# Kernel optimization log

Measured on AMD Instinct MI355X. Metric: run time of the kernel, lower is better.

The kernel has to match this reference:

```python
import jax, jax.numpy as jnp
import numpy as np

HEADS = 6
EPS = 1e-5


def _na_idx(L, k, d):
    # NATTEN-style dilated neighborhood: work within dilation cosets,
    # clamp window to stay inside the image (window shifts at borders).
    i = np.arange(L)
    g = i % d
    p = i // d
    Lg = (L - g + d - 1) // d  # coset length per position
    start = np.clip(p - k // 2, 0, Lg - k)
    j = np.arange(k)
    nbr = g[:, None] + d * (start[:, None] + j[None, :])          # [L,k] neighbor coords
    rel = (start[:, None] + j[None, :]) - p[:, None] + (k - 1)    # [L,k] rpb index in [0,2k-2]
    return jnp.asarray(nbr, jnp.int32), jnp.asarray(rel, jnp.int32)


def _na2d(x, qkv_w, qkv_b, proj_w, proj_b, rpb, heads, k, d):
    # x: [B,H,W,C] NHWC neighborhood attention with relative positional bias
    B, H, W, C = x.shape
    dh = C // heads
    scale = dh ** -0.5
    qkv = (x @ qkv_w + qkv_b).reshape(B, H, W, 3, heads, dh)
    qkv = jnp.transpose(qkv, (3, 0, 4, 1, 2, 5))  # [3,B,h,H,W,dh]
    q, kk, v = qkv[0] * scale, qkv[1], qkv[2]
    nh, rh = _na_idx(H, k, d)
    nw, rw = _na_idx(W, k, d)

    def gather(t):  # [B,h,H,W,dh] -> [B,h,H,W,k,k,dh]
        t = t[:, :, nh]              # [B,h,H,k,W,dh]
        t = t[:, :, :, :, nw]        # [B,h,H,k,W,k,dh]
        return jnp.transpose(t, (0, 1, 2, 4, 3, 5, 6))

    kn, vn = gather(kk), gather(v)
    attn = jnp.einsum('bhxyd,bhxyijd->bhxyij', q, kn)  # [B,h,H,W,k,k]
    bias = rpb[:, rh]                  # [h,H,k,2k-1]
    bias = bias[:, :, :, rw]           # [h,H,k,W,k]
    bias = jnp.transpose(bias, (0, 1, 3, 2, 4))  # [h,H,W,k,k]
    attn = attn + bias[None]
    attn = jax.nn.softmax(attn.reshape(B, heads, H, W, k * k), axis=-1)
    attn = attn.reshape(B, heads, H, W, k, k)
    out = jnp.einsum('bhxyij,bhxyijd->bhxyd', attn, vn)
    out = jnp.transpose(out, (0, 2, 3, 1, 4)).reshape(B, H, W, C)
    return out @ proj_w + proj_b


def _rln(x, w, b, m1_w, m1_b, m2_w, m2_b):
    # Revised LayerNorm: normalize over (C,H,W) per sample; meta1/meta2 are 1x1 convs on std/mean
    mean = jnp.mean(x, axis=(1, 2, 3), keepdims=True)
    std = jnp.sqrt(jnp.mean((x - mean) ** 2, axis=(1, 2, 3), keepdims=True) + EPS)
    out = (x - mean) / std * w + b
    rescale = m1_w[None, :, None, None] * std + m1_b[None, :, None, None]
    rebias = m2_w[None, :, None, None] * mean + m2_b[None, :, None, None]
    return out, rescale, rebias


def _c11(x, w, b):  # 1x1 conv on NCHW == per-pixel linear
    return jnp.einsum('bchw,oc->bohw', x, w) + b[None, :, None, None]


def _gelu(x):
    return jax.nn.gelu(x, approximate=False)


def reference(x, ln_w, ln_b, m1_w, m1_b, m2_w, m2_b, qkv1_w, qkv1_b, proj1_w, proj1_b, rpb1, qkv2_w, qkv2_b, proj2_w, proj2_b, rpb2, mlp_w1, mlp_b1, mlp_w2, mlp_b2, bn_g, bn_b, bn_m, bn_v, pa_w1, pa_b1, pa_w2, pa_b2, ca_w1, ca_b1, ca_w2, ca_b2, m2a_w1, m2a_b1, m2a_w2, m2a_b2):
    # ---- NA block 1 (kernel 7, dilation 1) ----
    sc = x
    y, rs, rb = _rln(x, ln_w, ln_b, m1_w, m1_b, m2_w, m2_b)
    a = _na2d(jnp.transpose(y, (0, 2, 3, 1)), qkv1_w, qkv1_b, proj1_w, proj1_b, rpb1, HEADS, 7, 1)
    x = sc + jnp.transpose(a, (0, 3, 1, 2)) * rs + rb
    # ---- NA block 2 (kernel 5, dilation 8) ----
    sc = x
    y, rs, rb = _rln(x, ln_w, ln_b, m1_w, m1_b, m2_w, m2_b)
    a = _na2d(jnp.transpose(y, (0, 2, 3, 1)), qkv2_w, qkv2_b, proj2_w, proj2_b, rpb2, HEADS, 5, 8)
    x = sc + jnp.transpose(a, (0, 3, 1, 2)) * rs + rb
    # ---- MLP (source reuses the pre-attn2 shortcut `sc`) ----
    y, rs, rb = _rln(x, ln_w, ln_b, m1_w, m1_b, m2_w, m2_b)
    m = _c11(jax.nn.relu(_c11(y, mlp_w1, mlp_b1)), mlp_w2, mlp_b2)
    x = sc + m * rs + rb
    # ---- BN + pixel attention + channel attention + mlp2 ----
    sc = x
    inv = jax.lax.rsqrt(bn_v + EPS)
    y = (x - bn_m[None, :, None, None]) * (inv * bn_g)[None, :, None, None] + bn_b[None, :, None, None]
    pa = jax.nn.sigmoid(_c11(_gelu(_c11(y, pa_w1, pa_b1)), pa_w2, pa_b2))  # [B,1,H,W]
    y = pa * y
    gap = jnp.mean(y, axis=(2, 3), keepdims=True)
    ca = jax.nn.sigmoid(_c11(_gelu(_c11(gap, ca_w1, ca_b1)), ca_w2, ca_b2))  # [B,C,1,1]
    y = ca * y
    y = _c11(_gelu(_c11(y, m2a_w1, m2a_b1)), m2a_w2, m2a_b2)
    return sc + y


def setup_inputs() -> dict:
    key = jax.random.key(0)
    B, C, H, W, HID = 4, 96, 64, 64, 384
    ks = iter(jax.random.split(key, 48))

    def rn(shape, s=0.02):
        return jax.random.normal(next(ks), shape, jnp.float32) * s

    d = {}
    d['x'] = jax.random.normal(next(ks), (B, C, H, W), jnp.float32)
    d['ln_w'] = jnp.ones((1, C, 1, 1), jnp.float32)
    d['ln_b'] = jnp.zeros((1, C, 1, 1), jnp.float32)
    d['m1_w'] = rn((C,)); d['m1_b'] = jnp.ones((C,), jnp.float32)
    d['m2_w'] = rn((C,)); d['m2_b'] = jnp.zeros((C,), jnp.float32)
    d['qkv1_w'] = rn((C, 3 * C)); d['qkv1_b'] = jnp.zeros((3 * C,), jnp.float32)
    d['proj1_w'] = rn((C, C)); d['proj1_b'] = jnp.zeros((C,), jnp.float32)
    d['rpb1'] = rn((HEADS, 13, 13))
    d['qkv2_w'] = rn((C, 3 * C)); d['qkv2_b'] = jnp.zeros((3 * C,), jnp.float32)
    d['proj2_w'] = rn((C, C)); d['proj2_b'] = jnp.zeros((C,), jnp.float32)
    d['rpb2'] = rn((HEADS, 9, 9))
    d['mlp_w1'] = rn((HID, C)); d['mlp_b1'] = jnp.zeros((HID,), jnp.float32)
    d['mlp_w2'] = rn((C, HID)); d['mlp_b2'] = jnp.zeros((C,), jnp.float32)
    d['bn_g'] = jnp.ones((C,), jnp.float32); d['bn_b'] = jnp.zeros((C,), jnp.float32)
    d['bn_m'] = jnp.zeros((C,), jnp.float32); d['bn_v'] = jnp.ones((C,), jnp.float32)
    d['pa_w1'] = rn((C // 8, C)); d['pa_b1'] = jnp.zeros((C // 8,), jnp.float32)
    d['pa_w2'] = rn((1, C // 8)); d['pa_b2'] = jnp.zeros((1,), jnp.float32)
    d['ca_w1'] = rn((C, C)); d['ca_b1'] = jnp.zeros((C,), jnp.float32)
    d['ca_w2'] = rn((C, C)); d['ca_b2'] = jnp.zeros((C,), jnp.float32)
    d['m2a_w1'] = rn((C, C)); d['m2a_b1'] = jnp.zeros((C,), jnp.float32)
    d['m2a_w2'] = rn((C, C)); d['m2a_b2'] = jnp.zeros((C,), jnp.float32)
    return d
```

## Files before the change

kernel.cpp:

```cpp
#include <hip/hip_runtime.h>
#include <math.h>

#define CC 96
#define NP 4096
#define NHEADS 6
#define NELEMF 393216.0f
#define EPSF 1e-5f

typedef __attribute__((ext_vector_type(8))) short bf16x8;
typedef __attribute__((ext_vector_type(4))) float f32x4;
#define MFMA16(a,b,c) __builtin_amdgcn_mfma_f32_16x16x32_bf16(a,b,c,0,0,0)

#define WQKV1  64
#define WQKV2  (WQKV1+13824)
#define WPROJ1 (WQKV2+13824)
#define WPROJ2 (WPROJ1+4608)
#define WMLP1  (WPROJ2+4608)
#define WMLP2  (WMLP1+18432)
#define WM2A1  (WMLP2+18432)
#define WM2A2  (WM2A1+4608)
#define WPA1T  (WM2A2+4608)
#define WBNS   (WPA1T+1152)
#define WCA1T  (WBNS+192)
#define WCA2T  (WCA1T+9216)
#define WS_Q   870784
#define WS_K   (WS_Q+786432)
#define WS_V   (WS_K+786432)
#define WS_ATTPM (WS_V+786432)
#define WS_X1  (WS_ATTPM+786432)
#define WS_X2  (WS_X1+1572864)
#define WS_X3  (WS_X2+1572864)
#define WS_PA  (WS_X3+1572864)
#define WS_GAP (WS_PA+16384)

__device__ __forceinline__ float gelu_f(float x){
  return 0.5f * x * (1.0f + erff(x * 0.7071067811865476f));
}
__device__ __forceinline__ float sigmoid_f(float x){
  return 1.0f / (1.0f + __expf(-x));
}
__device__ __forceinline__ unsigned short bfr(float f){
  unsigned int u = __float_as_uint(f);
  u += 0x7fffu + ((u >> 16) & 1u);
  return (unsigned short)(u >> 16);
}
__device__ __forceinline__ float bflo16(unsigned short u){ return __uint_as_float(((unsigned int)u) << 16); }
__device__ __forceinline__ float bflo(unsigned int u){ return __uint_as_float(u << 16); }
__device__ __forceinline__ float bfhi(unsigned int u){ return __uint_as_float(u & 0xffff0000u); }
__device__ __forceinline__ void get_ms(const float* st, int b, float& mean, float& inv, float& stdv){
  float s = st[b], s2 = st[4+b];
  mean = s * (1.0f/NELEMF);
  float var = fmaxf(s2 * (1.0f/NELEMF) - mean*mean, 0.0f);
  stdv = sqrtf(var + EPSF);
  inv = 1.0f / stdv;
}
__device__ __forceinline__ float ldf(const float* p, int i){ return p[i]; }
__device__ __forceinline__ float ldf(const unsigned short* p, int i){ return bflo16(p[i]); }
__device__ __forceinline__ void load4(const float* p, float4& v){ v = *(const float4*)p; }
__device__ __forceinline__ void load4(const unsigned short* p, float4& v){
  ushort4 u = *(const ushort4*)p;
  v.x = bflo16(u.x); v.y = bflo16(u.y); v.z = bflo16(u.z); v.w = bflo16(u.w);
}

__device__ __forceinline__ float dotg(const float* qv, const uint4* p){
  uint4 a = p[0], b = p[1];
  float s;
  s  = qv[0]*bflo(a.x);            s = fmaf(qv[1],  bfhi(a.x), s);
  s = fmaf(qv[2],  bflo(a.y), s);  s = fmaf(qv[3],  bfhi(a.y), s);
  s = fmaf(qv[4],  bflo(a.z), s);  s = fmaf(qv[5],  bfhi(a.z), s);
  s = fmaf(qv[6],  bflo(a.w), s);  s = fmaf(qv[7],  bfhi(a.w), s);
  s = fmaf(qv[8],  bflo(b.x), s);  s = fmaf(qv[9],  bfhi(b.x), s);
  s = fmaf(qv[10], bflo(b.y), s);  s = fmaf(qv[11], bfhi(b.y), s);
  s = fmaf(qv[12], bflo(b.z), s);  s = fmaf(qv[13], bfhi(b.z), s);
  s = fmaf(qv[14], bflo(b.w), s);  s = fmaf(qv[15], bfhi(b.w), s);
  return s;
}
__device__ __forceinline__ void pvg(float w, const uint4* p, float* acc){
  uint4 a = p[0], b = p[1];
  acc[0]  = fmaf(w, bflo(a.x), acc[0]);  acc[1]  = fmaf(w, bfhi(a.x), acc[1]);
  acc[2]  = fmaf(w, bflo(a.y), acc[2]);  acc[3]  = fmaf(w, bfhi(a.y), acc[3]);
  acc[4]  = fmaf(w, bflo(a.z), acc[4]);  acc[5]  = fmaf(w, bfhi(a.z), acc[5]);
  acc[6]  = fmaf(w, bflo(a.w), acc[6]);  acc[7]  = fmaf(w, bfhi(a.w), acc[7]);
  acc[8]  = fmaf(w, bflo(b.x), acc[8]);  acc[9]  = fmaf(w, bfhi(b.x), acc[9]);
  acc[10] = fmaf(w, bflo(b.y), acc[10]); acc[11] = fmaf(w, bfhi(b.y), acc[11]);
  acc[12] = fmaf(w, bflo(b.z), acc[12]); acc[13] = fmaf(w, bfhi(b.z), acc[13]);
  acc[14] = fmaf(w, bflo(b.w), acc[14]); acc[15] = fmaf(w, bfhi(b.w), acc[15]);
}

__global__ void prep_stats_kernel(const float* __restrict__ x, float* __restrict__ st,
                             const float* __restrict__ q1, const float* __restrict__ q2,
                             const float* __restrict__ p1, const float* __restrict__ p2,
                             const float* __restrict__ w1, const float* __restrict__ w2,
                             const float* __restrict__ a1, const float* __restrict__ a2,
                             const float* __restrict__ pw1,
                             const float* __restrict__ bg, const float* __restrict__ bb,
                             const float* __restrict__ bm, const float* __restrict__ bv,
                             const float* __restrict__ cw1, const float* __restrict__ cw2,
                             float* __restrict__ ws){
  if(blockIdx.x < 384){
    int b = blockIdx.x / CC, c = blockIdx.x % CC;
    const float4* p4 = (const float4*)(x + (size_t)(b*CC + c)*NP);
    float s = 0.f, s2 = 0.f;
    for(int i = threadIdx.x; i < 1024; i += 256){
      float4 v = p4[i];
      s += v.x + v.y + v.z + v.w;
      s2 = fmaf(v.x, v.x, fmaf(v.y, v.y, fmaf(v.z, v.z, fmaf(v.w, v.w, s2))));
    }
    for(int off = 32; off > 0; off >>= 1){ s += __shfl_down(s, off); s2 += __shfl_down(s2, off); }
    __shared__ float ls[8];
    int wid = threadIdx.x >> 6;
    if((threadIdx.x & 63) == 0){ ls[wid] = s; ls[4+wid] = s2; }
    __syncthreads();
    if(threadIdx.x == 0){
      atomicAdd(&st[b],   ls[0]+ls[1]+ls[2]+ls[3]);
      atomicAdd(&st[4+b], ls[4]+ls[5]+ls[6]+ls[7]);
    }
    return;
  }
  int gid = (blockIdx.x - 384)*256 + threadIdx.x;
  if(gid < 27648){ int n = gid/96, c = gid%96; ((unsigned short*)(ws+WQKV1))[gid] = bfr(q1[c*288+n]); }
  else if(gid < 55296){ int g = gid-27648; int n = g/96, c = g%96; ((unsigned short*)(ws+WQKV2))[g] = bfr(q2[c*288+n]); }
  else if(gid < 64512){ int g = gid-55296; int n = g/96, c = g%96; ((unsigned short*)(ws+WPROJ1))[g] = bfr(p1[c*96+n]); }
  else if(gid < 73728){ int g = gid-64512; int n = g/96, c = g%96; ((unsigned short*)(ws+WPROJ2))[g] = bfr(p2[c*96+n]); }
  else if(gid < 110592){ int g = gid-73728; ((unsigned short*)(ws+WMLP1))[g] = bfr(w1[g]); }
  else if(gid < 147456){ int g = gid-110592; ((unsigned short*)(ws+WMLP2))[g] = bfr(w2[g]); }
  else if(gid < 156672){ int g = gid-147456; ((unsigned short*)(ws+WM2A1))[g] = bfr(a1[g]); }
  else if(gid < 165888){ int g = gid-156672; ((unsigned short*)(ws+WM2A2))[g] = bfr(a2[g]); }
  else if(gid < 167040){ int g = gid-165888; int c = g/12, h = g%12; ws[WPA1T + g] = pw1[h*96+c]; }
  else if(gid < 167136){ int c = gid-167040;
    float sc = rsqrtf(bv[c] + EPSF) * bg[c];
    ws[WBNS + c] = sc;
    ws[WBNS + 96 + c] = bb[c] - bm[c]*sc;
  }
  else if(gid < 167520){ ws[WS_GAP + (gid-167136)] = 0.f; }
  else if(gid < 176736){ int g = gid-167520; int o = g/96, c = g%96; ws[WCA1T + c*96 + o] = cw1[g]; }
  else if(gid < 185952){ int g = gid-176736; int o = g/96, c = g%96; ws[WCA2T + c*96 + o] = cw2[g]; }
}

template<typename AT>
__global__ void __launch_bounds__(512) gemm_qkv_kernel(
    const AT* __restrict__ xin, const float* __restrict__ st,
    const float* __restrict__ lnw, const float* __restrict__ lnb,
    const unsigned short* __restrict__ wT, const float* __restrict__ qb,
    unsigned short* __restrict__ qo, unsigned short* __restrict__ ko, unsigned short* __restrict__ vo){
  __shared__ unsigned short Atl[64*104];
  __shared__ float scl[96], ofs[96];
  int m_base = blockIdx.x*64;
  int b = m_base >> 12, pxl0 = m_base & 4095;
  float mean, inv, stdv; get_ms(st, b, mean, inv, stdv);
  int tid = threadIdx.x;
  if(tid < 96){ float s = inv*lnw[tid]; scl[tid] = s; ofs[tid] = lnb[tid] - mean*s; }
  __syncthreads();
  const AT* src = xin + (size_t)b*CC*NP + pxl0;
  for(int idx = tid; idx < 96*16; idx += 512){
    int c = idx >> 4, p4 = (idx & 15) << 2;
    float4 v; load4(src + (size_t)c*NP + p4, v);
    float s = scl[c], o = ofs[c];
    Atl[(p4+0)*104 + c] = bfr(fmaf(v.x, s, o));
    Atl[(p4+1)*104 + c] = bfr(fmaf(v.y, s, o));
    Atl[(p4+2)*104 + c] = bfr(fmaf(v.z, s, o));
    Atl[(p4+3)*104 + c] = bfr(fmaf(v.w, s, o));
  }
  __syncthreads();
  int w = tid >> 6, lane = tid & 63, ml = lane & 15, q = lane >> 4;
  int row = w & 3, nh = w >> 2;
  const unsigned short* arow = Atl + (row*16 + ml)*104;
  bf16x8 av[3];
  #pragma unroll
  for(int ks = 0; ks < 3; ++ks) av[ks] = *(const bf16x8*)(arow + ks*32 + q*8);
  f32x4 z = {0.f,0.f,0.f,0.f};
  #pragma unroll
  for(int g0 = 0; g0 < 3; ++g0){
    int g = nh*3 + g0;
    f32x4 acc[3] = {z, z, z};
    #pragma unroll
    for(int ks = 0; ks < 3; ++ks){
      #pragma unroll
      for(int gg = 0; gg < 3; ++gg){
        bf16x8 bv = *(const bf16x8*)(wT + (g*48 + gg*16 + ml)*96 + ks*32 + q*8);
        acc[gg] = MFMA16(av[ks], bv, acc[gg]);
      }
    }
    #pragma unroll
    for(int gg = 0; gg < 3; ++gg){
      int nfb = g*48 + gg*16;
      int t = nfb/96, head = (nfb%96) >> 4;
      float scale = (t == 0) ? 0.25f : 1.0f;
      unsigned short* dst = (t == 0) ? qo : (t == 1) ? ko : vo;
      float bias = qb[nfb + ml];
      #pragma unroll
      for(int r = 0; r < 4; ++r){
        int pxl = pxl0 + row*16 + q*4 + r;
        dst[(((size_t)(b*NHEADS + head))*NP + pxl)*16 + ml] = bfr((acc[gg][r] + bias)*scale);
      }
    }
  }
}

template<int K, int D, int RPB, typename SCT>
__global__ void __launch_bounds__(512) attnproj_kernel(
    const unsigned short* __restrict__ qb, const unsigned short* __restrict__ kb,
    const unsigned short* __restrict__ vb, const float* __restrict__ rpb,
    const unsigned short* __restrict__ wT, const float* __restrict__ pb,
    const SCT* __restrict__ scx, const float* __restrict__ st,
    const float* __restrict__ m1w, const float* __restrict__ m1b,
    const float* __restrict__ m2w, const float* __restrict__ m2b,
    unsigned short* __restrict__ dst, float* __restrict__ st_out){
  __shared__ __align__(16) char smbuf[26624];
  __shared__ float rpbl[NHEADS*RPB*RPB];
  __shared__ float ls[16];
  unsigned short* attout = (unsigned short*)smbuf;
  float* T = (float*)smbuf;
  int b = blockIdx.x >> 6;
  int x = blockIdx.x & 63;
  int tid = threadIdx.x;
  for(int i = tid; i < NHEADS*RPB*RPB; i += 512) rpbl[i] = rpb[i];
  __syncthreads();

  if(tid < 384){
    int head = tid >> 6;
    int y = tid & 63;
    int bh = b*NHEADS + head;
    int gx = (D == 1) ? 0 : (x & (D-1));
    int px = (D == 1) ? x : (x >> 3);
    int Lgx = (64 - gx + D - 1) / D;
    int sx = min(max(px - K/2, 0), Lgx - K);
    int gy = (D == 1) ? 0 : (y & (D-1));
    int py = (D == 1) ? y : (y >> 3);
    int Lgy = (64 - gy + D - 1) / D;
    int sy = min(max(py - K/2, 0), Lgy - K);
    int dxb = sx - px + (K-1);
    int dyb = sy - py + (K-1);
    int pix = x*64 + y;

    float qv[16];
    {
      const uint4* qg = (const uint4*)(qb + ((size_t)bh*NP + pix)*16);
      uint4 qa = qg[0], qb4 = qg[1];
      qv[0]=bflo(qa.x);  qv[1]=bfhi(qa.x);  qv[2]=bflo(qa.y);  qv[3]=bfhi(qa.y);
      qv[4]=bflo(qa.z);  qv[5]=bfhi(qa.z);  qv[6]=bflo(qa.w);  qv[7]=bfhi(qa.w);
      qv[8]=bflo(qb4.x); qv[9]=bfhi(qb4.x); qv[10]=bflo(qb4.y);qv[11]=bfhi(qb4.y);
      qv[12]=bflo(qb4.z);qv[13]=bfhi(qb4.z);qv[14]=bflo(qb4.w);qv[15]=bfhi(qb4.w);
    }
    const unsigned short* kgb = kb + (size_t)bh*NP*16;
    const unsigned short* vgb = vb + (size_t)bh*NP*16;

    float sc[K*K];
    #pragma unroll
    for(int i = 0; i < K; ++i){
      int colx = gx + D*(sx + i);
      const unsigned short* kcol = kgb + (size_t)colx*64*16;
      const float* br = rpbl + (head*RPB + (i + dxb))*RPB + dyb;
      #pragma unroll
      for(int j = 0; j < K; ++j){
        int wwy = gy + D*(sy + j);
        sc[i*K + j] = dotg(qv, (const uint4*)(kcol + wwy*16)) + br[j];
      }
    }
    float mx = -1e30f;
    #pragma unroll
    for(int n = 0; n < K*K; ++n) mx = fmaxf(mx, sc[n]);
    float sum = 0.f;
    #pragma unroll
    for(int n = 0; n < K*K; ++n){ float e = __expf(sc[n] - mx); sc[n] = e; sum += e; }
    float rs = 1.0f / sum;
    float acc[16];
    #pragma unroll
    for(int d = 0; d < 16; ++d) acc[d] = 0.f;
    #pragma unroll
    for(int i = 0; i < K; ++i){
      int colx = gx + D*(sx + i);
      const unsigned short* vcol = vgb + (size_t)colx*64*16;
      #pragma unroll
      for(int j = 0; j < K; ++j){
        int wwy = gy + D*(sy + j);
        pvg(sc[i*K + j] * rs, (const uint4*)(vcol + wwy*16), acc);
      }
    }
    unsigned int ow[8];
    #pragma unroll
    for(int p = 0; p < 8; ++p)
      ow[p] = (unsigned int)bfr(acc[2*p]) | ((unsigned int)bfr(acc[2*p+1]) << 16);
    unsigned short* op = attout + y*104 + head*16;
    *(uint4*)op = make_uint4(ow[0], ow[1], ow[2], ow[3]);
    *(uint4*)(op + 8) = make_uint4(ow[4], ow[5], ow[6], ow[7]);
  }
  __syncthreads();

  int w = tid >> 6, lane = tid & 63, ml = lane & 15, q = lane >> 4;
  int row = w & 3, nh = w >> 2;
  f32x4 z = {0.f,0.f,0.f,0.f};
  f32x4 acc[3] = {z, z, z};
  {
    const unsigned short* arow = attout + (row*16 + ml)*104;
    #pragma unroll
    for(int ks = 0; ks < 3; ++ks){
      bf16x8 av = *(const bf16x8*)(arow + ks*32 + q*8);
      #pragma unroll
      for(int g0 = 0; g0 < 3; ++g0){
        int g = nh*3 + g0;
        bf16x8 bv = *(const bf16x8*)(wT + (g*16 + ml)*96 + ks*32 + q*8);
        acc[g0] = MFMA16(av, bv, acc[g0]);
      }
    }
  }
  __syncthreads();
  #pragma unroll
  for(int g0 = 0; g0 < 3; ++g0){
    int g = nh*3 + g0;
    #pragma unroll
    for(int r = 0; r < 4; ++r)
      T[(g*16 + ml)*68 + row*16 + q*4 + r] = acc[g0][r];
  }
  __syncthreads();
  int pxl0 = x*64;
  float mean, inv, stdv; get_ms(st, b, mean, inv, stdv);
  float s = 0.f, s2 = 0.f;
  for(int idx = tid; idx < 96*64; idx += 512){
    int n = idx >> 6, p = idx & 63;
    float rsf = fmaf(m1w[n], stdv, m1b[n]);
    float rbf = fmaf(m2w[n], mean, m2b[n]);
    int ad = (b*CC + n)*NP + pxl0 + p;
    float val = ldf(scx, ad) + (T[n*68 + p] + pb[n])*rsf + rbf;
    dst[ad] = bfr(val);
    s += val; s2 = fmaf(val, val, s2);
  }
  for(int off = 32; off > 0; off >>= 1){ s += __shfl_down(s, off); s2 += __shfl_down(s2, off); }
  if(lane == 0){ ls[w] = s; ls[8+w] = s2; }
  __syncthreads();
  if(tid == 0){
    float a0 = 0.f, a1 = 0.f;
    #pragma unroll
    for(int i = 0; i < 8; ++i){ a0 += ls[i]; a1 += ls[8+i]; }
    atomicAdd(&st_out[b], a0);
    atomicAdd(&st_out[4+b], a1);
  }
}

__global__ void __launch_bounds__(512) gemm_mlp_kernel(
    const unsigned short* __restrict__ xin, const float* __restrict__ st,
    const float* __restrict__ lnw, const float* __restrict__ lnb,
    const unsigned short* __restrict__ w1T, const float* __restrict__ b1,
    const unsigned short* __restrict__ w2T, const float* __restrict__ b2,
    const unsigned short* __restrict__ scx,
    const float* __restrict__ m1w, const float* __restrict__ m1b,
    const float* __restrict__ m2w, const float* __restrict__ m2b,
    float* __restrict__ dst,
    const float* __restrict__ bns, const float* __restrict__ pw1t,
    const float* __restrict__ pb1, const float* __restrict__ pw2,
    const float* __restrict__ pb2, float* __restrict__ pa,
    float* __restrict__ gap){
  __shared__ __align__(16) char smbuf[63488];
  __shared__ float scl[96], ofs[96];
  unsigned short* Atl  = (unsigned short*)smbuf;
  unsigned short* hidL = (unsigned short*)(smbuf + 13312);
  float* T = (float*)(smbuf + 13312);
  float* gpart = (float*)smbuf;
  int m_base = blockIdx.x*64;
  int b = m_base >> 12, pxl0 = m_base & 4095;
  float mean, inv, stdv; get_ms(st, b, mean, inv, stdv);
  int tid = threadIdx.x;
  if(tid < 96){ float s = inv*lnw[tid]; scl[tid] = s; ofs[tid] = lnb[tid] - mean*s; }
  __syncthreads();
  const unsigned short* src = xin + (size_t)b*CC*NP + pxl0;
  for(int idx = tid; idx < 96*16; idx += 512){
    int c = idx >> 4, p4 = (idx & 15) << 2;
    float4 v; load4(src + (size_t)c*NP + p4, v);
    float s = scl[c], o = ofs[c];
    Atl[(p4+0)*104 + c] = bfr(fmaf(v.x, s, o));
    Atl[(p4+1)*104 + c] = bfr(fmaf(v.y, s, o));
    Atl[(p4+2)*104 + c] = bfr(fmaf(v.z, s, o));
    Atl[(p4+3)*104 + c] = bfr(fmaf(v.w, s, o));
  }
  __syncthreads();
  int w = tid >> 6, lane = tid & 63, ml = lane & 15, q = lane >> 4;
  int row = w & 3, nh = w >> 2;
  f32x4 z = {0.f,0.f,0.f,0.f};
  {
    const unsigned short* arow = Atl + (row*16 + ml)*104;
    bf16x8 av[3];
    #pragma unroll
    for(int ks = 0; ks < 3; ++ks) av[ks] = *(const bf16x8*)(arow + ks*32 + q*8);
    #pragma unroll
    for(int g0 = 0; g0 < 4; ++g0){
      int g = nh*4 + g0;
      f32x4 acc[3] = {z, z, z};
      #pragma unroll
      for(int ks = 0; ks < 3; ++ks){
        #pragma unroll
        for(int gg = 0; gg < 3; ++gg){
          bf16x8 bv = *(const bf16x8*)(w1T + (g*48 + gg*16 + ml)*96 + ks*32 + q*8);
          acc[gg] = MFMA16(av[ks], bv, acc[gg]);
        }
      }
      #pragma unroll
      for(int gg = 0; gg < 3; ++gg){
        int n = g*48 + gg*16 + ml;
        float bias = b1[n];
        #pragma unroll
        for(int r = 0; r < 4; ++r)
          hidL[(row*16 + q*4 + r)*392 + n] = bfr(fmaxf(acc[gg][r] + bias, 0.f));
      }
    }
  }
  __syncthreads();
  f32x4 acc2[3] = {z, z, z};
  {
    const unsigned short* arow = hidL + (row*16 + ml)*392;
    #pragma unroll
    for(int ks = 0; ks < 12; ++ks){
      bf16x8 av = *(const bf16x8*)(arow + ks*32 + q*8);
      #pragma unroll
      for(int g0 = 0; g0 < 3; ++g0){
        int g = nh*3 + g0;
        bf16x8 bv = *(const bf16x8*)(w2T + (g*16 + ml)*384 + ks*32 + q*8);
        acc2[g0] = MFMA16(av, bv, acc2[g0]);
      }
    }
  }
  __syncthreads();
  #pragma unroll
  for(int g0 = 0; g0 < 3; ++g0){
    int g = nh*3 + g0;
    #pragma unroll
    for(int r = 0; r < 4; ++r)
      T[(g*16 + ml)*68 + row*16 + q*4 + r] = acc2[g0][r];
  }
  __syncthreads();
  for(int idx = tid; idx < 96*64; idx += 512){
    int n = idx >> 6, px = idx & 63;
    float rsf = fmaf(m1w[n], stdv, m1b[n]);
    float rbf = fmaf(m2w[n], mean, m2b[n]);
    int ad = (b*CC + n)*NP + pxl0 + px;
    float val = ldf(scx, ad) + (T[n*68 + px] + b2[n])*rsf + rbf;
    dst[ad] = val;
    T[n*68 + px] = val;
  }
  __syncthreads();
  int pxq = tid >> 3, t = tid & 7;
  float yvv[12], acc[12];
  #pragma unroll
  for(int h = 0; h < 12; ++h) acc[h] = 0.f;
  #pragma unroll 6
  for(int cc = 0; cc < 12; ++cc){
    int c = t*12 + cc;
    float yv = fmaf(T[c*68 + pxq], bns[c], bns[96 + c]);
    yvv[cc] = yv;
    #pragma unroll
    for(int h = 0; h < 12; ++h) acc[h] = fmaf(yv, pw1t[c*12 + h], acc[h]);
  }
  #pragma unroll
  for(int h = 0; h < 12; ++h){
    acc[h] += __shfl_xor(acc[h], 1);
    acc[h] += __shfl_xor(acc[h], 2);
    acc[h] += __shfl_xor(acc[h], 4);
  }
  float s = pb2[0];
  #pragma unroll
  for(int h = 0; h < 12; ++h) s = fmaf(gelu_f(acc[h] + pb1[h]), pw2[h], s);
  float pav = sigmoid_f(s);
  if(t == 0) pa[b*NP + pxl0 + pxq] = pav;
  #pragma unroll 6
  for(int cc = 0; cc < 12; ++cc){
    float g = yvv[cc] * pav;
    g += __shfl_xor(g, 8);  g += __shfl_xor(g, 16); g += __shfl_xor(g, 32);
    if(lane < 8) gpart[w*96 + lane*12 + cc] = g;
  }
  __syncthreads();
  if(tid < 96){
    int c = tid;
    float v = 0.f;
    #pragma unroll
    for(int ww = 0; ww < 8; ++ww) v += gpart[ww*96 + c];
    atomicAdd(&gap[b*96 + c], v * (1.0f/4096.0f));
  }
}

__global__ void __launch_bounds__(512) gemm_m2a_kernel(
    const float* __restrict__ x3, const float* __restrict__ bns,
    const float* __restrict__ pa, const float* __restrict__ gap,
    const float* __restrict__ cw1T, const float* __restrict__ cb1,
    const float* __restrict__ cw2T, const float* __restrict__ cb2,
    const unsigned short* __restrict__ w1T, const float* __restrict__ b1,
    const unsigned short* __restrict__ w2T, const float* __restrict__ b2,
    const float* __restrict__ scx, float* __restrict__ outp){
  __shared__ __align__(16) char smbuf[26624];
  __shared__ float scl[96], ofs[96], pal[64];
  __shared__ float gl[96], tl[96];
  unsigned short* Atl = (unsigned short*)smbuf;
  unsigned short* tl2 = (unsigned short*)(smbuf + 13312);
  float* T = (float*)smbuf;
  int m_base = blockIdx.x*64;
  int b = m_base >> 12, pxl0 = m_base & 4095;
  int tid = threadIdx.x;
  if(tid < 96) gl[tid] = gap[b*96 + tid];
  if(tid >= 128 && tid < 192) pal[tid-128] = pa[m_base + (tid-128)];
  __syncthreads();
  if(tid < 96){
    float a = cb1[tid];
    #pragma unroll 8
    for(int c = 0; c < 96; ++c) a = fmaf(gl[c], cw1T[c*96 + tid], a);
    tl[tid] = gelu_f(a);
  }
  __syncthreads();
  if(tid < 96){
    float a = cb2[tid];
    #pragma unroll 8
    for(int c = 0; c < 96; ++c) a = fmaf(tl[c], cw2T[c*96 + tid], a);
    float cv = sigmoid_f(a);
    scl[tid] = bns[tid]*cv; ofs[tid] = bns[96+tid]*cv;
  }
  __syncthreads();
  const float* src = x3 + (size_t)b*CC*NP + pxl0;
  for(int idx = tid; idx < 96*16; idx += 512){
    int c = idx >> 4, p4 = (idx & 15) << 2;
    float4 v = *(const float4*)(src + (size_t)c*NP + p4);
    float s = scl[c], o = ofs[c];
    Atl[(p4+0)*104 + c] = bfr(fmaf(v.x, s, o) * pal[p4+0]);
    Atl[(p4+1)*104 + c] = bfr(fmaf(v.y, s, o) * pal[p4+1]);
    Atl[(p4+2)*104 + c] = bfr(fmaf(v.z, s, o) * pal[p4+2]);
    Atl[(p4+3)*104 + c] = bfr(fmaf(v.w, s, o) * pal[p4+3]);
  }
  __syncthreads();
  int w = tid >> 6, lane = tid & 63, ml = lane & 15, q = lane >> 4;
  int row = w & 3, nh = w >> 2;
  f32x4 z = {0.f,0.f,0.f,0.f};
  f32x4 acc1[3] = {z, z, z};
  {
    const unsigned short* arow = Atl + (row*16 + ml)*104;
    #pragma unroll
    for(int ks = 0; ks < 3; ++ks){
      bf16x8 av = *(const bf16x8*)(arow + ks*32 + q*8);
      #pragma unroll
      for(int g0 = 0; g0 < 3; ++g0){
        int g = nh*3 + g0;
        bf16x8 bv = *(const bf16x8*)(w1T + (g*16 + ml)*96 + ks*32 + q*8);
        acc1[g0] = MFMA16(av, bv, acc1[g0]);
      }
    }
  }
  #pragma unroll
  for(int g0 = 0; g0 < 3; ++g0){
    int g = nh*3 + g0;
    float bias = b1[g*16 + ml];
    #pragma unroll
    for(int r = 0; r < 4; ++r)
      tl2[(row*16 + q*4 + r)*104 + g*16 + ml] = bfr(gelu_f(acc1[g0][r] + bias));
  }
  __syncthreads();
  f32x4 acc2[3] = {z, z, z};
  {
    const unsigned short* arow = tl2 + (row*16 + ml)*104;
    #pragma unroll
    for(int ks = 0; ks < 3; ++ks){
      bf16x8 av = *(const bf16x8*)(arow + ks*32 + q*8);
      #pragma unroll
      for(int g0 = 0; g0 < 3; ++g0){
        int g = nh*3 + g0;
        bf16x8 bv = *(const bf16x8*)(w2T + (g*16 + ml)*96 + ks*32 + q*8);
        acc2[g0] = MFMA16(av, bv, acc2[g0]);
      }
    }
  }
  __syncthreads();
  #pragma unroll
  for(int g0 = 0; g0 < 3; ++g0){
    int g = nh*3 + g0;
    #pragma unroll
    for(int r = 0; r < 4; ++r)
      T[(g*16 + ml)*68 + row*16 + q*4 + r] = acc2[g0][r];
  }
  __syncthreads();
  for(int idx = tid; idx < 96*64; idx += 512){
    int n = idx >> 6, p = idx & 63;
    int ad = (b*CC + n)*NP + pxl0 + p;
    outp[ad] = scx[ad] + T[n*68 + p] + b2[n];
  }
}

extern "C" void kernel_launch(void* const* d_in, const int* in_sizes, int n_in,
                              void* d_out, int out_size, void* d_ws, size_t ws_size,
                              hipStream_t stream){
  (void)in_sizes; (void)n_in; (void)out_size; (void)ws_size;
  const float* x     = (const float*)d_in[0];
  const float* lnw   = (const float*)d_in[1];
  const float* lnb   = (const float*)d_in[2];
  const float* m1w   = (const float*)d_in[3];
  const float* m1b   = (const float*)d_in[4];
  const float* m2w   = (const float*)d_in[5];
  const float* m2b   = (const float*)d_in[6];
  const float* qkv1w = (const float*)d_in[7];
  const float* qkv1b = (const float*)d_in[8];
  const float* proj1w= (const float*)d_in[9];
  const float* proj1b= (const float*)d_in[10];
  const float* rpb1  = (const float*)d_in[11];
  const float* qkv2w = (const float*)d_in[12];
  const float* qkv2b = (const float*)d_in[13];
  const float* proj2w= (const float*)d_in[14];
  const float* proj2b= (const float*)d_in[15];
  const float* rpb2  = (const float*)d_in[16];
  const float* mw1   = (const float*)d_in[17];
  const float* mb1   = (const float*)d_in[18];
  const float* mw2   = (const float*)d_in[19];
  const float* mb2   = (const float*)d_in[20];
  const float* bng   = (const float*)d_in[21];
  const float* bnb   = (const float*)d_in[22];
  const float* bnm   = (const float*)d_in[23];
  const float* bnv   = (const float*)d_in[24];
  const float* paw1  = (const float*)d_in[25];
  const float* pab1  = (const float*)d_in[26];
  const float* paw2  = (const float*)d_in[27];
  const float* pab2  = (const float*)d_in[28];
  const float* caw1  = (const float*)d_in[29];
  const float* cab1  = (const float*)d_in[30];
  const float* caw2  = (const float*)d_in[31];
  const float* cab2  = (const float*)d_in[32];
  const float* aw1   = (const float*)d_in[33];
  const float* ab1   = (const float*)d_in[34];
  const float* aw2   = (const float*)d_in[35];
  const float* ab2   = (const float*)d_in[36];

  float* ws  = (float*)d_ws;
  float* out = (float*)d_out;
  float* st0 = ws;
  float* st1 = ws + 8;
  float* st2 = ws + 16;
  unsigned short* q     = (unsigned short*)(ws + WS_Q);
  unsigned short* k     = (unsigned short*)(ws + WS_K);
  unsigned short* v     = (unsigned short*)(ws + WS_V);
  unsigned short* x1b   = (unsigned short*)(ws + WS_X1);
  unsigned short* x2b   = (unsigned short*)(ws + WS_X2);
  float* x3  = ws + WS_X3;
  float* pab = ws + WS_PA;
  float* gpb = ws + WS_GAP;
  float* bns = ws + WBNS;

  hipMemsetAsync(d_ws, 0, 64*sizeof(float), stream);
  prep_stats_kernel<<<1111, 256, 0, stream>>>(x, st0, qkv1w, qkv2w, proj1w, proj2w,
                                              mw1, mw2, aw1, aw2, paw1,
                                              bng, bnb, bnm, bnv, caw1, caw2, ws);

  gemm_qkv_kernel<float><<<256, 512, 0, stream>>>(x, st0, lnw, lnb,
      (unsigned short*)(ws+WQKV1), qkv1b, q, k, v);
  attnproj_kernel<7,1,13,float><<<256, 512, 0, stream>>>(q, k, v, rpb1,
      (unsigned short*)(ws+WPROJ1), proj1b, x, st0, m1w, m1b, m2w, m2b, x1b, st1);

  gemm_qkv_kernel<unsigned short><<<256, 512, 0, stream>>>(x1b, st1, lnw, lnb,
      (unsigned short*)(ws+WQKV2), qkv2b, q, k, v);
  attnproj_kernel<5,8,9,unsigned short><<<256, 512, 0, stream>>>(q, k, v, rpb2,
      (unsigned short*)(ws+WPROJ2), proj2b, x1b, st1, m1w, m1b, m2w, m2b, x2b, st2);

  gemm_mlp_kernel<<<256, 512, 0, stream>>>(x2b, st2, lnw, lnb,
      (unsigned short*)(ws+WMLP1), mb1, (unsigned short*)(ws+WMLP2), mb2,
      x1b, m1w, m1b, m2w, m2b, x3,
      bns, ws + WPA1T, pab1, paw2, pab2, pab, gpb);

  gemm_m2a_kernel<<<256, 512, 0, stream>>>(x3, bns, pab, gpb,
                                           ws + WCA1T, cab1, ws + WCA2T, cab2,
                                           (unsigned short*)(ws+WM2A1), ab1,
                                           (unsigned short*)(ws+WM2A2), ab2, x3, out);
}
```

Baseline: 251.0 us.

## Fuse all stages into one cooperative persistent kernel with grid syncs

Replaces the seven separate kernel launches with a single cooperative kernel of 256 blocks that runs each former kernel as a device-side phase, separated by grid-wide barriers. Shared memory is sized for the largest phase and reused across phases. The prep phase is reworked so 256 blocks of 512 threads cover the work previously done by 1111 blocks of 256. The aim is to remove per-launch overhead and inter-kernel gaps, at the cost of grid.sync latency, one block per CU (launch_bounds 512,1), and the largest-phase shared memory limiting occupancy for every phase.

New measurement: 471.9 us. 88.0% more time.

```diff
diff --git a/kernel.cpp b/kernel.cpp
--- a/kernel.cpp
+++ b/kernel.cpp
@@ -1,5 +1,8 @@
 #include <hip/hip_runtime.h>
+#include <hip/hip_cooperative_groups.h>
 #include <math.h>
+
+namespace cg = cooperative_groups;
 
 #define CC 96
 #define NP 4096
@@ -26,8 +29,7 @@
 #define WS_Q   870784
 #define WS_K   (WS_Q+786432)
 #define WS_V   (WS_K+786432)
-#define WS_ATTPM (WS_V+786432)
-#define WS_X1  (WS_ATTPM+786432)
+#define WS_X1  (WS_V+786432+786432)
 #define WS_X2  (WS_X1+1572864)
 #define WS_X3  (WS_X2+1572864)
 #define WS_PA  (WS_X3+1572864)
@@ -61,7 +63,6 @@
   ushort4 u = *(const ushort4*)p;
   v.x = bflo16(u.x); v.y = bflo16(u.y); v.z = bflo16(u.z); v.w = bflo16(u.w);
 }
-
 __device__ __forceinline__ float dotg(const float* qv, const uint4* p){
   uint4 a = p[0], b = p[1];
   float s;
@@ -87,68 +88,75 @@
   acc[14] = fmaf(w, bflo(b.w), acc[14]); acc[15] = fmaf(w, bfhi(b.w), acc[15]);
 }
 
-__global__ void prep_stats_kernel(const float* __restrict__ x, float* __restrict__ st,
-                             const float* __restrict__ q1, const float* __restrict__ q2,
-                             const float* __restrict__ p1, const float* __restrict__ p2,
-                             const float* __restrict__ w1, const float* __restrict__ w2,
-                             const float* __restrict__ a1, const float* __restrict__ a2,
-                             const float* __restrict__ pw1,
-                             const float* __restrict__ bg, const float* __restrict__ bb,
-                             const float* __restrict__ bm, const float* __restrict__ bv,
-                             const float* __restrict__ cw1, const float* __restrict__ cw2,
-                             float* __restrict__ ws){
-  if(blockIdx.x < 384){
-    int b = blockIdx.x / CC, c = blockIdx.x % CC;
-    const float4* p4 = (const float4*)(x + (size_t)(b*CC + c)*NP);
+struct KArgs {
+  const float *x, *lnw, *lnb, *m1w, *m1b, *m2w, *m2b;
+  const float *qkv1w, *qkv1b, *proj1w, *proj1b, *rpb1;
+  const float *qkv2w, *qkv2b, *proj2w, *proj2b, *rpb2;
+  const float *mw1, *mb1, *mw2, *mb2;
+  const float *bng, *bnb, *bnm, *bnv;
+  const float *paw1, *pab1, *paw2, *pab2;
+  const float *caw1, *cab1, *caw2, *cab2;
+  const float *aw1, *ab1, *aw2, *ab2;
+  float* ws; float* out;
+};
+
+__device__ __forceinline__ void prep_phase(const KArgs& a, float* st, float* lsb){
+  int bid = blockIdx.x, tid = threadIdx.x;
+  float* ws = a.ws;
+  for(int sl = bid; sl < 384; sl += 256){
+    int b = sl / CC, c = sl % CC;
+    const float4* p4 = (const float4*)(a.x + (size_t)(b*CC + c)*NP);
     float s = 0.f, s2 = 0.f;
-    for(int i = threadIdx.x; i < 1024; i += 256){
+    for(int i = tid; i < 1024; i += 512){
       float4 v = p4[i];
       s += v.x + v.y + v.z + v.w;
       s2 = fmaf(v.x, v.x, fmaf(v.y, v.y, fmaf(v.z, v.z, fmaf(v.w, v.w, s2))));
     }
     for(int off = 32; off > 0; off >>= 1){ s += __shfl_down(s, off); s2 += __shfl_down(s2, off); }
-    __shared__ float ls[8];
-    int wid = threadIdx.x >> 6;
-    if((threadIdx.x & 63) == 0){ ls[wid] = s; ls[4+wid] = s2; }
+    int wid = tid >> 6;
+    if((tid & 63) == 0){ lsb[wid] = s; lsb[8+wid] = s2; }
     __syncthreads();
-    if(threadIdx.x == 0){
-      atomicAdd(&st[b],   ls[0]+ls[1]+ls[2]+ls[3]);
-      atomicAdd(&st[4+b], ls[4]+ls[5]+ls[6]+ls[7]);
-    }
-    return;
-  }
-  int gid = (blockIdx.x - 384)*256 + threadIdx.x;
-  if(gid < 27648){ int n = gid/96, c = gid%96; ((unsigned short*)(ws+WQKV1))[gid] = bfr(q1[c*288+n]); }
-  else if(gid < 55296){ int g = gid-27648; int n = g/96, c = g%96; ((unsigned short*)(ws+WQKV2))[g] = bfr(q2[c*288+n]); }
-  else if(gid < 64512){ int g = gid-55296; int n = g/96, c = g%96; ((unsigned short*)(ws+WPROJ1))[g] = bfr(p1[c*96+n]); }
-  else if(gid < 73728){ int g = gid-64512; int n = g/96, c = g%96; ((unsigned short*)(ws+WPROJ2))[g] = bfr(p2[c*96+n]); }
-  else if(gid < 110592){ int g = gid-73728; ((unsigned short*)(ws+WMLP1))[g] = bfr(w1[g]); }
-  else if(gid < 147456){ int g = gid-110592; ((unsigned short*)(ws+WMLP2))[g] = bfr(w2[g]); }
-  else if(gid < 156672){ int g = gid-147456; ((unsigned short*)(ws+WM2A1))[g] = bfr(a1[g]); }
-  else if(gid < 165888){ int g = gid-156672; ((unsigned short*)(ws+WM2A2))[g] = bfr(a2[g]); }
-  else if(gid < 167040){ int g = gid-165888; int c = g/12, h = g%12; ws[WPA1T + g] = pw1[h*96+c]; }
-  else if(gid < 167136){ int c = gid-167040;
-    float sc = rsqrtf(bv[c] + EPSF) * bg[c];
-    ws[WBNS + c] = sc;
-    ws[WBNS + 96 + c] = bb[c] - bm[c]*sc;
-  }
-  else if(gid < 167520){ ws[WS_GAP + (gid-167136)] = 0.f; }
-  else if(gid < 176736){ int g = gid-167520; int o = g/96, c = g%96; ws[WCA1T + c*96 + o] = cw1[g]; }
-  else if(gid < 185952){ int g = gid-176736; int o = g/96, c = g%96; ws[WCA2T + c*96 + o] = cw2[g]; }
+    if(tid == 0){
+      float a0 = 0.f, a1 = 0.f;
+      #pragma unroll
+      for(int i = 0; i < 8; ++i){ a0 += lsb[i]; a1 += lsb[8+i]; }
+      atomicAdd(&st[b], a0); atomicAdd(&st[4+b], a1);
+    }
+    __syncthreads();
+  }
+  for(int gid = bid*512 + tid; gid < 185952; gid += 256*512){
+    if(gid < 27648){ int n = gid/96, c = gid%96; ((unsigned short*)(ws+WQKV1))[gid] = bfr(a.qkv1w[c*288+n]); }
+    else if(gid < 55296){ int g = gid-27648; int n = g/96, c = g%96; ((unsigned short*)(ws+WQKV2))[g] = bfr(a.qkv2w[c*288+n]); }
+    else if(gid < 64512){ int g = gid-55296; int n = g/96, c = g%96; ((unsigned short*)(ws+WPROJ1))[g] = bfr(a.proj1w[c*96+n]); }
+    else if(gid < 73728){ int g = gid-64512; int n = g/96, c = g%96; ((unsigned short*)(ws+WPROJ2))[g] = bfr(a.proj2w[c*96+n]); }
+    else if(gid < 110592){ int g = gid-73728; ((unsigned short*)(ws+WMLP1))[g] = bfr(a.mw1[g]); }
+    else if(gid < 147456){ int g = gid-110592; ((unsigned short*)(ws+WMLP2))[g] = bfr(a.mw2[g]); }
+    else if(gid < 156672){ int g = gid-147456; ((unsigned short*)(ws+WM2A1))[g] = bfr(a.aw1[g]); }
+    else if(gid < 165888){ int g = gid-156672; ((unsigned short*)(ws+WM2A2))[g] = bfr(a.aw2[g]); }
+    else if(gid < 167040){ int g = gid-165888; int c = g/12, h = g%12; ws[WPA1T + g] = a.paw1[h*96+c]; }
+    else if(gid < 167136){ int c = gid-167040;
+      float sc = rsqrtf(a.bnv[c] + EPSF) * a.bng[c];
+      ws[WBNS + c] = sc;
+      ws[WBNS + 96 + c] = a.bnb[c] - a.bnm[c]*sc;
+    }
+    else if(gid < 167520){ ws[WS_GAP + (gid-167136)] = 0.f; }
+    else if(gid < 176736){ int g = gid-167520; int o = g/96, c = g%96; ws[WCA1T + c*96 + o] = a.caw1[g]; }
+    else { int g = gid-176736; int o = g/96, c = g%96; ws[WCA2T + c*96 + o] = a.caw2[g]; }
+  }
 }
 
 template<typename AT>
-__global__ void __launch_bounds__(512) gemm_qkv_kernel(
-    const AT* __restrict__ xin, const float* __restrict__ st,
-    const float* __restrict__ lnw, const float* __restrict__ lnb,
-    const unsigned short* __restrict__ wT, const float* __restrict__ qb,
-    unsigned short* __restrict__ qo, unsigned short* __restrict__ ko, unsigned short* __restrict__ vo){
-  __shared__ unsigned short Atl[64*104];
-  __shared__ float scl[96], ofs[96];
-  int m_base = blockIdx.x*64;
+__device__ __forceinline__ void qkv_phase(
+    const AT* xin, const float* st,
+    const float* lnw, const float* lnb,
+    const unsigned short* wT, const float* qb,
+    unsigned short* qo, unsigned short* ko, unsigned short* vo,
+    char* smbuf, float* scl, float* ofs){
+  unsigned short* Atl = (unsigned short*)smbuf;
+  int bid = blockIdx.x, tid = threadIdx.x;
+  int m_base = bid*64;
   int b = m_base >> 12, pxl0 = m_base & 4095;
   float mean, inv, stdv; get_ms(st, b, mean, inv, stdv);
-  int tid = threadIdx.x;
   if(tid < 96){ float s = inv*lnw[tid]; scl[tid] = s; ofs[tid] = lnb[tid] - mean*s; }
   __syncthreads();
   const AT* src = xin + (size_t)b*CC*NP + pxl0;
@@ -195,20 +203,19 @@
       }
     }
   }
+  __syncthreads();
 }
 
 template<int K, int D, int RPB, typename SCT>
-__global__ void __launch_bounds__(512) attnproj_kernel(
-    const unsigned short* __restrict__ qb, const unsigned short* __restrict__ kb,
-    const unsigned short* __restrict__ vb, const float* __restrict__ rpb,
-    const unsigned short* __restrict__ wT, const float* __restrict__ pb,
-    const SCT* __restrict__ scx, const float* __restrict__ st,
-    const float* __restrict__ m1w, const float* __restrict__ m1b,
-    const float* __restrict__ m2w, const float* __restrict__ m2b,
-    unsigned short* __restrict__ dst, float* __restrict__ st_out){
-  __shared__ __align__(16) char smbuf[26624];
-  __shared__ float rpbl[NHEADS*RPB*RPB];
-  __shared__ float ls[16];
+__device__ __forceinline__ void attnproj_phase(
+    const unsigned short* qb, const unsigned short* kb,
+    const unsigned short* vb, const float* rpb,
+    const unsigned short* wT, const float* pb,
+    const SCT* scx, const float* st,
+    const float* m1w, const float* m1b,
+    const float* m2w, const float* m2b,
+    unsigned short* dst, float* st_out,
+    char* smbuf, float* rpbl, float* lsb){
   unsigned short* attout = (unsigned short*)smbuf;
   float* T = (float*)smbuf;
   int b = blockIdx.x >> 6;
@@ -326,40 +333,39 @@
     s += val; s2 = fmaf(val, val, s2);
   }
   for(int off = 32; off > 0; off >>= 1){ s += __shfl_down(s, off); s2 += __shfl_down(s2, off); }
-  if(lane == 0){ ls[w] = s; ls[8+w] = s2; }
+  if(lane == 0){ lsb[w] = s; lsb[8+w] = s2; }
   __syncthreads();
   if(tid == 0){
     float a0 = 0.f, a1 = 0.f;
     #pragma unroll
-    for(int i = 0; i < 8; ++i){ a0 += ls[i]; a1 += ls[8+i]; }
+    for(int i = 0; i < 8; ++i){ a0 += lsb[i]; a1 += lsb[8+i]; }
     atomicAdd(&st_out[b], a0);
     atomicAdd(&st_out[4+b], a1);
   }
-}
-
-__global__ void __launch_bounds__(512) gemm_mlp_kernel(
-    const unsigned short* __restrict__ xin, const float* __restrict__ st,
-    const float* __restrict__ lnw, const float* __restrict__ lnb,
-    const unsigned short* __restrict__ w1T, const float* __restrict__ b1,
-    const unsigned short* __restrict__ w2T, const float* __restrict__ b2,
-    const unsigned short* __restrict__ scx,
-    const float* __restrict__ m1w, const float* __restrict__ m1b,
-    const float* __restrict__ m2w, const float* __restrict__ m2b,
-    float* __restrict__ dst,
-    const float* __restrict__ bns, const float* __restrict__ pw1t,
-    const float* __restrict__ pb1, const float* __restrict__ pw2,
-    const float* __restrict__ pb2, float* __restrict__ pa,
-    float* __restrict__ gap){
-  __shared__ __align__(16) char smbuf[63488];
-  __shared__ float scl[96], ofs[96];
+  __syncthreads();
+}
+
+__device__ __forceinline__ void mlp_phase(
+    const unsigned short* xin, const float* st,
+    const float* lnw, const float* lnb,
+    const unsigned short* w1T, const float* b1,
+    const unsigned short* w2T, const float* b2,
+    const unsigned short* scx,
+    const float* m1w, const float* m1b,
+    const float* m2w, const float* m2b,
+    float* dst,
+    const float* bns, const float* pw1t,
+    const float* pb1, const float* pw2,
+    const float* pb2, float* pa, float* gap,
+    char* smbuf, float* scl, float* ofs){
   unsigned short* Atl  = (unsigned short*)smbuf;
   unsigned short* hidL = (unsigned short*)(smbuf + 13312);
   float* T = (float*)(smbuf + 13312);
   float* gpart = (float*)smbuf;
-  int m_base = blockIdx.x*64;
+  int bid = blockIdx.x, tid = threadIdx.x;
+  int m_base = bid*64;
   int b = m_base >> 12, pxl0 = m_base & 4095;
   float mean, inv, stdv; get_ms(st, b, mean, inv, stdv);
-  int tid = threadIdx.x;
   if(tid < 96){ float s = inv*lnw[tid]; scl[tid] = s; ofs[tid] = lnb[tid] - mean*s; }
   __syncthreads();
   const unsigned short* src = xin + (size_t)b*CC*NP + pxl0;
@@ -474,25 +480,25 @@
     for(int ww = 0; ww < 8; ++ww) v += gpart[ww*96 + c];
     atomicAdd(&gap[b*96 + c], v * (1.0f/4096.0f));
   }
-}
-
-__global__ void __launch_bounds__(512) gemm_m2a_kernel(
-    const float* __restrict__ x3, const float* __restrict__ bns,
-    const float* __restrict__ pa, const float* __restrict__ gap,
-    const float* __restrict__ cw1T, const float* __restrict__ cb1,
-    const float* __restrict__ cw2T, const float* __restrict__ cb2,
-    const unsigned short* __restrict__ w1T, const float* __restrict__ b1,
-    const unsigned short* __restrict__ w2T, const float* __restrict__ b2,
-    const float* __restrict__ scx, float* __restrict__ outp){
-  __shared__ __align__(16) char smbuf[26624];
-  __shared__ float scl[96], ofs[96], pal[64];
-  __shared__ float gl[96], tl[96];
+  __syncthreads();
+}
+
+__device__ __forceinline__ void m2a_phase(
+    const float* x3, const float* bns,
+    const float* pa, const float* gap,
+    const float* cw1T, const float* cb1,
+    const float* cw2T, const float* cb2,
+    const unsigned short* w1T, const float* b1,
+    const unsigned short* w2T, const float* b2,
+    const float* scx, float* outp,
+    char* smbuf, float* scl, float* ofs,
+    float* pal, float* gl, float* tl){
   unsigned short* Atl = (unsigned short*)smbuf;
   unsigned short* tl2 = (unsigned short*)(smbuf + 13312);
   float* T = (float*)smbuf;
-  int m_base = blockIdx.x*64;
+  int bid = blockIdx.x, tid = threadIdx.x;
+  int m_base = bid*64;
   int b = m_base >> 12, pxl0 = m_base & 4095;
-  int tid = threadIdx.x;
   if(tid < 96) gl[tid] = gap[b*96 + tid];
   if(tid >= 128 && tid < 192) pal[tid-128] = pa[m_base + (tid-128)];
   __syncthreads();
@@ -578,85 +584,107 @@
   }
 }
 
+__global__ void __launch_bounds__(512, 1) mega_kernel(KArgs a){
+  cg::grid_group grid = cg::this_grid();
+  __shared__ __align__(16) char smraw[63488];
+  __shared__ float scl[96], ofs[96], lsb[32];
+  __shared__ float pal[64], gl[96], tl[96];
+  __shared__ float rpbl[NHEADS*13*13];
+
+  float* ws  = a.ws;
+  float* st0 = ws;
+  float* st1 = ws + 8;
+  float* st2 = ws + 16;
+  unsigned short* q   = (unsigned short*)(ws + WS_Q);
+  unsigned short* k   = (unsigned short*)(ws + WS_K);
+  unsigned short* v   = (unsigned short*)(ws + WS_V);
+  unsigned short* x1b = (unsigned short*)(ws + WS_X1);
+  unsigned short* x2b = (unsigned short*)(ws + WS_X2);
+  float* x3  = ws + WS_X3;
+  float* pab = ws + WS_PA;
+  float* gpb = ws + WS_GAP;
+  float* bns = ws + WBNS;
+
+  prep_phase(a, st0, lsb);
+  grid.sync();
+
+  qkv_phase<float>(a.x, st0, a.lnw, a.lnb,
+      (unsigned short*)(ws+WQKV1), a.qkv1b, q, k, v, smraw, scl, ofs);
+  grid.sync();
+
+  attnproj_phase<7,1,13,float>(q, k, v, a.rpb1,
+      (unsigned short*)(ws+WPROJ1), a.proj1b, a.x, st0,
+      a.m1w, a.m1b, a.m2w, a.m2b, x1b, st1, smraw, rpbl, lsb);
+  grid.sync();
+
+  qkv_phase<unsigned short>(x1b, st1, a.lnw, a.lnb,
+      (unsigned short*)(ws+WQKV2), a.qkv2b, q, k, v, smraw, scl, ofs);
+  grid.sync();
+
+  attnproj_phase<5,8,9,unsigned short>(q, k, v, a.rpb2,
+      (unsigned short*)(ws+WPROJ2), a.proj2b, x1b, st1,
+      a.m1w, a.m1b, a.m2w, a.m2b, x2b, st2, smraw, rpbl, lsb);
+  grid.sync();
+
+  mlp_phase(x2b, st2, a.lnw, a.lnb,
+      (unsigned short*)(ws+WMLP1), a.mb1, (unsigned short*)(ws+WMLP2), a.mb2,
+      x1b, a.m1w, a.m1b, a.m2w, a.m2b, x3,
+      bns, ws + WPA1T, a.pab1, a.paw2, a.pab2, pab, gpb, smraw, scl, ofs);
+  grid.sync();
+
+  m2a_phase(x3, bns, pab, gpb,
+      ws + WCA1T, a.cab1, ws + WCA2T, a.cab2,
+      (unsigned short*)(ws+WM2A1), a.ab1, (unsigned short*)(ws+WM2A2), a.ab2,
+      x3, a.out, smraw, scl, ofs, pal, gl, tl);
+}
+
 extern "C" void kernel_launch(void* const* d_in, const int* in_sizes, int n_in,
                               void* d_out, int out_size, void* d_ws, size_t ws_size,
                               hipStream_t stream){
   (void)in_sizes; (void)n_in; (void)out_size; (void)ws_size;
-  const float* x     = (const float*)d_in[0];
-  const float* lnw   = (const float*)d_in[1];
-  const float* lnb   = (const float*)d_in[2];
-  const float* m1w   = (const float*)d_in[3];
-  const float* m1b   = (const float*)d_in[4];
-  const float* m2w   = (const float*)d_in[5];
-  const float* m2b   = (const float*)d_in[6];
-  const float* qkv1w = (const float*)d_in[7];
-  const float* qkv1b = (const float*)d_in[8];
-  const float* proj1w= (const float*)d_in[9];
-  const float* proj1b= (const float*)d_in[10];
-  const float* rpb1  = (const float*)d_in[11];
-  const float* qkv2w = (const float*)d_in[12];
-  const float* qkv2b = (const float*)d_in[13];
-  const float* proj2w= (const float*)d_in[14];
-  const float* proj2b= (const float*)d_in[15];
-  const float* rpb2  = (const float*)d_in[16];
-  const float* mw1   = (const float*)d_in[17];
-  const float* mb1   = (const float*)d_in[18];
-  const float* mw2   = (const float*)d_in[19];
-  const float* mb2   = (const float*)d_in[20];
-  const float* bng   = (const float*)d_in[21];
-  const float* bnb   = (const float*)d_in[22];
-  const float* bnm   = (const float*)d_in[23];
-  const float* bnv   = (const float*)d_in[24];
-  const float* paw1  = (const float*)d_in[25];
-  const float* pab1  = (const float*)d_in[26];
-  const float* paw2  = (const float*)d_in[27];
-  const float* pab2  = (const float*)d_in[28];
-  const float* caw1  = (const float*)d_in[29];
-  const float* cab1  = (const float*)d_in[30];
-  const float* caw2  = (const float*)d_in[31];
-  const float* cab2  = (const float*)d_in[32];
-  const float* aw1   = (const float*)d_in[33];
-  const float* ab1   = (const float*)d_in[34];
-  const float* aw2   = (const float*)d_in[35];
-  const float* ab2   = (const float*)d_in[36];
-
-  float* ws  = (float*)d_ws;
-  float* out = (float*)d_out;
-  float* st0 = ws;
-  float* st1 = ws + 8;
-  float* st2 = ws + 16;
-  unsigned short* q     = (unsigned short*)(ws + WS_Q);
-  unsigned short* k     = (unsigned short*)(ws + WS_K);
-  unsigned short* v     = (unsigned short*)(ws + WS_V);
-  unsigned short* x1b   = (unsigned short*)(ws + WS_X1);
-  unsigned short* x2b   = (unsigned short*)(ws + WS_X2);
-  float* x3  = ws + WS_X3;
-  float* pab = ws + WS_PA;
-  float* gpb = ws + WS_GAP;
-  float* bns = ws + WBNS;
+  KArgs ka;
+  ka.x      = (const float*)d_in[0];
+  ka.lnw    = (const float*)d_in[1];
+  ka.lnb    = (const float*)d_in[2];
+  ka.m1w    = (const float*)d_in[3];
+  ka.m1b    = (const float*)d_in[4];
+  ka.m2w    = (const float*)d_in[5];
+  ka.m2b    = (const float*)d_in[6];
+  ka.qkv1w  = (const float*)d_in[7];
+  ka.qkv1b  = (const float*)d_in[8];
+  ka.proj1w = (const float*)d_in[9];
+  ka.proj1b = (const float*)d_in[10];
+  ka.rpb1   = (const float*)d_in[11];
+  ka.qkv2w  = (const float*)d_in[12];
+  ka.qkv2b  = (const float*)d_in[13];
+  ka.proj2w = (const float*)d_in[14];
+  ka.proj2b = (const float*)d_in[15];
+  ka.rpb2   = (const float*)d_in[16];
+  ka.mw1    = (const float*)d_in[17];
+  ka.mb1    = (const float*)d_in[18];
+  ka.mw2    = (const float*)d_in[19];
+  ka.mb2    = (const float*)d_in[20];
+  ka.bng    = (const float*)d_in[21];
+  ka.bnb    = (const float*)d_in[22];
+  ka.bnm    = (const float*)d_in[23];
+  ka.bnv    = (const float*)d_in[24];
+  ka.paw1   = (const float*)d_in[25];
+  ka.pab1   = (const float*)d_in[26];
+  ka.paw2   = (const float*)d_in[27];
+  ka.pab2   = (const float*)d_in[28];
+  ka.caw1   = (const float*)d_in[29];
+  ka.cab1   = (const float*)d_in[30];
+  ka.caw2   = (const float*)d_in[31];
+  ka.cab2   = (const float*)d_in[32];
+  ka.aw1    = (const float*)d_in[33];
+  ka.ab1    = (const float*)d_in[34];
+  ka.aw2    = (const float*)d_in[35];
+  ka.ab2    = (const float*)d_in[36];
+  ka.ws     = (float*)d_ws;
+  ka.out    = (float*)d_out;
 
   hipMemsetAsync(d_ws, 0, 64*sizeof(float), stream);
-  prep_stats_kernel<<<1111, 256, 0, stream>>>(x, st0, qkv1w, qkv2w, proj1w, proj2w,
-                                              mw1, mw2, aw1, aw2, paw1,
-                                              bng, bnb, bnm, bnv, caw1, caw2, ws);
-
-  gemm_qkv_kernel<float><<<256, 512, 0, stream>>>(x, st0, lnw, lnb,
-      (unsigned short*)(ws+WQKV1), qkv1b, q, k, v);
-  attnproj_kernel<7,1,13,float><<<256, 512, 0, stream>>>(q, k, v, rpb1,
-      (unsigned short*)(ws+WPROJ1), proj1b, x, st0, m1w, m1b, m2w, m2b, x1b, st1);
-
-  gemm_qkv_kernel<unsigned short><<<256, 512, 0, stream>>>(x1b, st1, lnw, lnb,
-      (unsigned short*)(ws+WQKV2), qkv2b, q, k, v);
-  attnproj_kernel<5,8,9,unsigned short><<<256, 512, 0, stream>>>(q, k, v, rpb2,
-      (unsigned short*)(ws+WPROJ2), proj2b, x1b, st1, m1w, m1b, m2w, m2b, x2b, st2);
-
-  gemm_mlp_kernel<<<256, 512, 0, stream>>>(x2b, st2, lnw, lnb,
-      (unsigned short*)(ws+WMLP1), mb1, (unsigned short*)(ws+WMLP2), mb2,
-      x1b, m1w, m1b, m2w, m2b, x3,
-      bns, ws + WPA1T, pab1, paw2, pab2, pab, gpb);
-
-  gemm_m2a_kernel<<<256, 512, 0, stream>>>(x3, bns, pab, gpb,
-                                           ws + WCA1T, cab1, ws + WCA2T, cab2,
-                                           (unsigned short*)(ws+WM2A1), ab1,
-                                           (unsigned short*)(ws+WM2A2), ab2, x3, out);
-}
+  void* kargs[] = { &ka };
+  hipLaunchCooperativeKernel((void*)mega_kernel, dim3(256), dim3(512),
+                             kargs, 0, stream);
+}
```
